# Kernel tuning notes

Hardware: AMD Instinct MI355X
Metric: run time of the kernel (lower is better)

## Reference

```python
import jax, jax.numpy as jnp
import numpy as np

NUM_EMBEDDINGS = 1024
EMBEDDING_DIM = 64
COMMITMENT_COST = 0.25


def setup_inputs() -> dict:
    key = jax.random.key(0)
    k1, k2 = jax.random.split(key)
    z = jax.random.normal(k1, (16, EMBEDDING_DIM, 64, 64), dtype=jnp.float32)
    # nn.Embedding init: uniform(-1/K, 1/K)
    emb = jax.random.uniform(
        k2, (NUM_EMBEDDINGS, EMBEDDING_DIM), dtype=jnp.float32,
        minval=-1.0 / NUM_EMBEDDINGS, maxval=1.0 / NUM_EMBEDDINGS)
    return {"z": z, "emb": emb}


def reference(z, emb):
    # b c h w -> b h w c
    zc = jnp.transpose(z, (0, 2, 3, 1))
    B, H, W, D = zc.shape
    zf = zc.reshape(-1, D)  # [N, D]
    K = emb.shape[0]

    # L2 distances: ||z||^2 + ||e||^2 - 2 z e^T   -> [N, K]
    distances = (jnp.sum(zf * zf, axis=1, keepdims=True)
                 + jnp.sum(emb * emb, axis=1)
                 - 2.0 * jnp.matmul(zf, emb.T))
    encoding_indices = jnp.argmin(distances, axis=1)  # [N]

    # one_hot @ emb  ==  gather
    quantized = emb[encoding_indices].reshape(zc.shape)  # [B,H,W,D]

    reconstruction_errors = jnp.sum((quantized - zc) ** 2, axis=-1).reshape(-1)
    avg_error = jnp.mean(reconstruction_errors)

    e_latent_loss = jnp.mean((jax.lax.stop_gradient(quantized) - zc) ** 2)
    q_latent_loss = jnp.mean((quantized - jax.lax.stop_gradient(zc)) ** 2)
    loss = q_latent_loss + COMMITMENT_COST * e_latent_loss

    # straight-through estimator
    quantized_st = zc + jax.lax.stop_gradient(quantized - zc)
    out = jnp.transpose(quantized_st, (0, 3, 1, 2))  # b h w c -> b c h w

    # perplexity: avg one-hot usage (histogram instead of dense one-hot)
    N = zf.shape[0]
    counts = jnp.zeros((K,), dtype=jnp.float32).at[encoding_indices].add(1.0)
    avg_probs = counts / N
    perplexity = jnp.exp(-jnp.sum(avg_probs * jnp.log(avg_probs + 1e-10)))

    return out, loss, perplexity, avg_error
```

## Files before the change

### kernel.cpp

```cpp
#include <hip/hip_runtime.h>
#include <stdint.h>

#define HW   4096
#define NEMB 1024

typedef float        f32x4  __attribute__((ext_vector_type(4)));
typedef short        h16x8  __attribute__((ext_vector_type(8)));
typedef unsigned int u32x4  __attribute__((ext_vector_type(4)));

#define CVTPKH(D, LO, HI) asm("v_cvt_pkrtz_f16_f32 %0, %1, %2" : "=v"(D) : "v"(LO), "v"(HI))

__device__ __forceinline__ void gload_lds16(const float* g, float* l) {
    __builtin_amdgcn_global_load_lds(
        (const __attribute__((address_space(1))) void*)(uintptr_t)g,
        (__attribute__((address_space(3))) void*)(uintptr_t)l, 16, 0, 0);
}

__global__ __launch_bounds__(128) void vq_init(const float* __restrict__ emb,
                                               unsigned int* __restrict__ counts,
                                               float* __restrict__ errsum,
                                               float* __restrict__ ens,
                                               unsigned int* __restrict__ embw) {
    const int k = blockIdx.x * 128 + threadIdx.x;
    counts[k] = 0u;
    if (k == 0) *errsum = 0.0f;
    const float* e = emb + k * 64;
    float a[8] = {0,0,0,0,0,0,0,0};
    unsigned int* dst = embw + k * 32;
    #pragma unroll
    for (int c = 0; c < 8; ++c) {
        f32x4 v0 = *(const f32x4*)(e + c * 8);
        f32x4 v1 = *(const f32x4*)(e + c * 8 + 4);
        a[0] += v0.x * v0.x; a[1] += v0.y * v0.y;
        a[2] += v0.z * v0.z; a[3] += v0.w * v0.w;
        a[4] += v1.x * v1.x; a[5] += v1.y * v1.y;
        a[6] += v1.z * v1.z; a[7] += v1.w * v1.w;
        u32x4 w;
        CVTPKH(w.x, v0.x, v0.y); CVTPKH(w.y, v0.z, v0.w);
        CVTPKH(w.z, v1.x, v1.y); CVTPKH(w.w, v1.z, v1.w);
        *(u32x4*)&dst[(c ^ (k & 7)) << 2] = w;
    }
    ens[k] = ((a[0]+a[1]) + (a[2]+a[3])) + ((a[4]+a[5]) + (a[6]+a[7]));
}

__global__ __launch_bounds__(512, 4)
void vq_main(const float* __restrict__ z, const float* __restrict__ emb,
             const float* __restrict__ ens, const unsigned int* __restrict__ embw,
             float* __restrict__ out, unsigned int* __restrict__ counts,
             float* __restrict__ errsum)
{
    __shared__ __attribute__((aligned(16))) float z_lds[64 * 128];
    __shared__ __attribute__((aligned(16))) unsigned int et_w[256 * 32];
    __shared__ __attribute__((aligned(16))) float ens_lds[NEMB];
    __shared__ int   idx_sh[128];
    __shared__ float errp[512];

    const int t   = threadIdx.x;
    const int n0  = blockIdx.x * 128;
    const int bb  = n0 >> 12;
    const int hw0 = n0 & 4095;
    const float* zb = z + bb * (64 * HW) + hw0;

    #pragma unroll
    for (int it = 0; it < 4; ++it) {
        const int p = it * 512 + t;
        gload_lds16(zb + (p >> 5) * HW + (p & 31) * 4, z_lds + p * 4);
    }
    if (t < 256) gload_lds16(ens + t * 4, ens_lds + t * 4);
    #pragma unroll
    for (int it = 0; it < 4; ++it) {
        const int p = it * 512 + t;
        gload_lds16((const float*)embw + p * 4, (float*)et_w + p * 4);
    }
    __syncthreads();

    const int l   = t & 63;
    const int wv  = t >> 6;
    const int col = l & 15;
    const int bg  = l >> 4;

    h16x8 a0, a1;
    {
        const int xs = wv * 16 + col;
        u32x4 wa, wb;
        #pragma unroll
        for (int p2 = 0; p2 < 4; ++p2) {
            float lo = z_lds[(bg * 8 + p2 * 2    ) * 128 + xs];
            float hi = z_lds[(bg * 8 + p2 * 2 + 1) * 128 + xs];
            CVTPKH(wa[p2], lo, hi);
            float lo2 = z_lds[(32 + bg * 8 + p2 * 2    ) * 128 + xs];
            float hi2 = z_lds[(32 + bg * 8 + p2 * 2 + 1) * 128 + xs];
            CVTPKH(wb[p2], lo2, hi2);
        }
        a0 = __builtin_bit_cast(h16x8, wa);
        a1 = __builtin_bit_cast(h16x8, wb);
    }

    const int slot0 = bg ^ (col & 7);
    const unsigned int* ep0 = et_w + col * 32 + slot0 * 4;
    const unsigned int* ep1 = et_w + col * 32 + (slot0 ^ 4) * 4;
    const float* ensp = ens_lds + col;

    float mval[4] = {__builtin_inff(), __builtin_inff(), __builtin_inff(), __builtin_inff()};
    int   midx[4] = {0, 0, 0, 0};

    #pragma unroll
    for (int kt = 0; kt < 4; ++kt) {
        #pragma unroll
        for (int i = 0; i < 16; ++i) {
            u32x4 bw0 = *(const u32x4*)(ep0 + i * 512);
            u32x4 bw1 = *(const u32x4*)(ep1 + i * 512);
            float en = ensp[kt * 256 + i * 16];
            f32x4 cc = {0.0f, 0.0f, 0.0f, 0.0f};
            cc = __builtin_amdgcn_mfma_f32_16x16x32_f16(a0, __builtin_bit_cast(h16x8, bw0), cc, 0, 0, 0);
            cc = __builtin_amdgcn_mfma_f32_16x16x32_f16(a1, __builtin_bit_cast(h16x8, bw1), cc, 0, 0, 0);
            const int kg = kt * 256 + i * 16 + col;
            #pragma unroll
            for (int j = 0; j < 4; ++j) {
                const float s = fmaf(-2.0f, cc[j], en);
                if (s < mval[j]) { mval[j] = s; midx[j] = kg; }
            }
        }

        __syncthreads();
        if (kt < 3) {
            const float* src = (const float*)(embw + (kt + 1) * 8192);
            #pragma unroll
            for (int it = 0; it < 4; ++it) {
                const int p = it * 512 + t;
                gload_lds16(src + p * 4, (float*)et_w + p * 4);
            }
            __syncthreads();
        }
    }

    #pragma unroll
    for (int j = 0; j < 4; ++j) {
        float m = mval[j]; int id = midx[j];
        #pragma unroll
        for (int mk = 1; mk <= 8; mk <<= 1) {
            float m2 = __shfl_xor(m, mk, 64);
            int   i2 = __shfl_xor(id, mk, 64);
            if (m2 < m || (m2 == m && i2 < id)) { m = m2; id = i2; }
        }
        if (col == 0) idx_sh[wv * 16 + bg * 4 + j] = id;
    }
    __syncthreads();

    if (t < 128) atomicAdd(&counts[idx_sh[t]], 1u);

    {
        const int x  = t & 127;
        const int cg = t >> 7;
        const int idx = idx_sh[x];
        const float* er = emb + idx * 64;
        float* ob = out + bb * (64 * HW) + hw0 + x;
        float part = 0.0f;
        #pragma unroll
        for (int cq = 0; cq < 4; ++cq) {
            const int c = cg * 16 + cq * 4;
            f32x4 e4 = *(const f32x4*)&er[c];
            float z0 = z_lds[(c+0) * 128 + x];
            float z1 = z_lds[(c+1) * 128 + x];
            float z2 = z_lds[(c+2) * 128 + x];
            float z3 = z_lds[(c+3) * 128 + x];
            ob[(c+0) * HW] = z0 + (e4.x - z0);
            ob[(c+1) * HW] = z1 + (e4.y - z1);
            ob[(c+2) * HW] = z2 + (e4.z - z2);
            ob[(c+3) * HW] = z3 + (e4.w - z3);
            float d0 = z0 - e4.x, d1 = z1 - e4.y, d2 = z2 - e4.z, d3 = z3 - e4.w;
            part = fmaf(d0, d0, part); part = fmaf(d1, d1, part);
            part = fmaf(d2, d2, part); part = fmaf(d3, d3, part);
        }
        errp[t] = part;
    }
    __syncthreads();
    if (t < 128) {
        float s = (errp[t] + errp[t + 128]) + (errp[t + 256] + errp[t + 384]);
        #pragma unroll
        for (int off = 32; off >= 1; off >>= 1) s += __shfl_down(s, off, 64);
        if ((t & 63) == 0) atomicAdd(errsum, s);
    }
}

__global__ __launch_bounds__(256) void vq_fin(const unsigned int* __restrict__ counts,
                                              const float* __restrict__ errsum,
                                              float* __restrict__ scal)
{
    __shared__ float part[4];
    const int t = threadIdx.x;
    float s = 0.0f;
    for (int k = t; k < NEMB; k += 256) {
        float p = (float)counts[k] * (1.0f / 65536.0f);
        s += p * logf(p + 1e-10f);
    }
    #pragma unroll
    for (int off = 32; off >= 1; off >>= 1) s += __shfl_down(s, off, 64);
    if ((t & 63) == 0) part[t >> 6] = s;
    __syncthreads();
    if (t == 0) {
        float tot = (part[0] + part[1]) + (part[2] + part[3]);
        float es  = *errsum;
        scal[0] = 1.25f * (es * (1.0f / 4194304.0f));
        scal[1] = expf(-tot);
        scal[2] = es * (1.0f / 65536.0f);
    }
}

extern "C" void kernel_launch(void* const* d_in, const int* in_sizes, int n_in,
                              void* d_out, int out_size, void* d_ws, size_t ws_size,
                              hipStream_t stream) {
    const float* z   = (const float*)d_in[0];
    const float* emb = (const float*)d_in[1];
    float* out = (float*)d_out;
    unsigned int* counts = (unsigned int*)d_ws;
    float* errsum = (float*)((char*)d_ws + 4096);
    float* ens    = (float*)((char*)d_ws + 8192);
    unsigned int* embw = (unsigned int*)((char*)d_ws + 16384);

    vq_init<<<8, 128, 0, stream>>>(emb, counts, errsum, ens, embw);
    vq_main<<<512, 512, 0, stream>>>(z, emb, ens, embw, out, counts, errsum);
    vq_fin<<<1, 256, 0, stream>>>(counts, errsum, out + 4194304);
}
```

Before: 46.95 us.

## Keep codebook slice in registers per wave and pack argmin into integer keys

Measured after the change: 44.13 us. 1.06x faster.

```diff
diff --git a/kernel.cpp b/kernel.cpp
--- a/kernel.cpp
+++ b/kernel.cpp
@@ -19,14 +19,14 @@
 __global__ __launch_bounds__(128) void vq_init(const float* __restrict__ emb,
                                                unsigned int* __restrict__ counts,
                                                float* __restrict__ errsum,
-                                               float* __restrict__ ens,
-                                               unsigned int* __restrict__ embw) {
+                                               float* __restrict__ ens1,
+                                               unsigned int* __restrict__ embh) {
     const int k = blockIdx.x * 128 + threadIdx.x;
     counts[k] = 0u;
     if (k == 0) *errsum = 0.0f;
     const float* e = emb + k * 64;
+    unsigned int* dst = embh + k * 32;
     float a[8] = {0,0,0,0,0,0,0,0};
-    unsigned int* dst = embw + k * 32;
     #pragma unroll
     for (int c = 0; c < 8; ++c) {
         f32x4 v0 = *(const f32x4*)(e + c * 8);
@@ -38,20 +38,21 @@
         u32x4 w;
         CVTPKH(w.x, v0.x, v0.y); CVTPKH(w.y, v0.z, v0.w);
         CVTPKH(w.z, v1.x, v1.y); CVTPKH(w.w, v1.z, v1.w);
-        *(u32x4*)&dst[(c ^ (k & 7)) << 2] = w;
-    }
-    ens[k] = ((a[0]+a[1]) + (a[2]+a[3])) + ((a[4]+a[5]) + (a[6]+a[7]));
+        *(u32x4*)&dst[c * 4] = w;
+    }
+    ens1[k] = 1.0f + (((a[0]+a[1]) + (a[2]+a[3])) + ((a[4]+a[5]) + (a[6]+a[7])));
 }
 
 __global__ __launch_bounds__(512, 4)
 void vq_main(const float* __restrict__ z, const float* __restrict__ emb,
-             const float* __restrict__ ens, const unsigned int* __restrict__ embw,
+             const float* __restrict__ ens1, const unsigned int* __restrict__ embh,
              float* __restrict__ out, unsigned int* __restrict__ counts,
              float* __restrict__ errsum)
 {
     __shared__ __attribute__((aligned(16))) float z_lds[64 * 128];
-    __shared__ __attribute__((aligned(16))) unsigned int et_w[256 * 32];
+    __shared__ __attribute__((aligned(16))) unsigned int zh[128 * 32];
     __shared__ __attribute__((aligned(16))) float ens_lds[NEMB];
+    __shared__ unsigned int kd[8][128];
     __shared__ int   idx_sh[128];
     __shared__ float errp[512];
 
@@ -66,88 +67,103 @@
         const int p = it * 512 + t;
         gload_lds16(zb + (p >> 5) * HW + (p & 31) * 4, z_lds + p * 4);
     }
-    if (t < 256) gload_lds16(ens + t * 4, ens_lds + t * 4);
-    #pragma unroll
-    for (int it = 0; it < 4; ++it) {
-        const int p = it * 512 + t;
-        gload_lds16((const float*)embw + p * 4, (float*)et_w + p * 4);
-    }
-    __syncthreads();
+    if (t < 256) gload_lds16(ens1 + t * 4, ens_lds + t * 4);
+    __syncthreads();
+
+    {
+        const int x = t & 127;
+        #pragma unroll
+        for (int ss = 0; ss < 2; ++ss) {
+            const int s = (x + (t >> 7) * 2 + ss) & 7;
+            const int c = s ^ (x & 7);
+            u32x4 w;
+            CVTPKH(w.x, z_lds[(8*c + 0) * 128 + x], z_lds[(8*c + 1) * 128 + x]);
+            CVTPKH(w.y, z_lds[(8*c + 2) * 128 + x], z_lds[(8*c + 3) * 128 + x]);
+            CVTPKH(w.z, z_lds[(8*c + 4) * 128 + x], z_lds[(8*c + 5) * 128 + x]);
+            CVTPKH(w.w, z_lds[(8*c + 6) * 128 + x], z_lds[(8*c + 7) * 128 + x]);
+            *(u32x4*)&zh[x * 32 + s * 4] = w;
+        }
+    }
 
     const int l   = t & 63;
     const int wv  = t >> 6;
     const int col = l & 15;
     const int bg  = l >> 4;
 
-    h16x8 a0, a1;
+    u32x4 bw0[8], bw1[8];
     {
-        const int xs = wv * 16 + col;
-        u32x4 wa, wb;
-        #pragma unroll
-        for (int p2 = 0; p2 < 4; ++p2) {
-            float lo = z_lds[(bg * 8 + p2 * 2    ) * 128 + xs];
-            float hi = z_lds[(bg * 8 + p2 * 2 + 1) * 128 + xs];
-            CVTPKH(wa[p2], lo, hi);
-            float lo2 = z_lds[(32 + bg * 8 + p2 * 2    ) * 128 + xs];
-            float hi2 = z_lds[(32 + bg * 8 + p2 * 2 + 1) * 128 + xs];
-            CVTPKH(wb[p2], lo2, hi2);
-        }
-        a0 = __builtin_bit_cast(h16x8, wa);
-        a1 = __builtin_bit_cast(h16x8, wb);
-    }
-
-    const int slot0 = bg ^ (col & 7);
-    const unsigned int* ep0 = et_w + col * 32 + slot0 * 4;
-    const unsigned int* ep1 = et_w + col * 32 + (slot0 ^ 4) * 4;
-    const float* ensp = ens_lds + col;
-
-    float mval[4] = {__builtin_inff(), __builtin_inff(), __builtin_inff(), __builtin_inff()};
-    int   midx[4] = {0, 0, 0, 0};
-
-    #pragma unroll
-    for (int kt = 0; kt < 4; ++kt) {
-        #pragma unroll
-        for (int i = 0; i < 16; ++i) {
-            u32x4 bw0 = *(const u32x4*)(ep0 + i * 512);
-            u32x4 bw1 = *(const u32x4*)(ep1 + i * 512);
-            float en = ensp[kt * 256 + i * 16];
+        const unsigned int* ebase = embh + (wv * 128 + col) * 32 + bg * 4;
+        #pragma unroll
+        for (int g = 0; g < 8; ++g) {
+            bw0[g] = *(const u32x4*)(ebase + g * 16 * 32);
+            bw1[g] = *(const u32x4*)(ebase + g * 16 * 32 + 16);
+        }
+    }
+    float en[8];
+    #pragma unroll
+    for (int g = 0; g < 8; ++g) en[g] = ens_lds[wv * 128 + g * 16 + col];
+
+    __syncthreads();
+
+    const unsigned int lkc = (unsigned int)col;
+    #pragma unroll 1
+    for (int st = 0; st < 8; ++st) {
+        const int xs = st * 16 + col;
+        const int sA = bg ^ (col & 7);
+        u32x4 wa = *(const u32x4*)&zh[xs * 32 + sA * 4];
+        u32x4 wb = *(const u32x4*)&zh[xs * 32 + (sA ^ 4) * 4];
+        h16x8 a0 = __builtin_bit_cast(h16x8, wa);
+        h16x8 a1 = __builtin_bit_cast(h16x8, wb);
+
+        unsigned int k0 = ~0u, k1 = ~0u, k2 = ~0u, k3 = ~0u;
+        #pragma unroll
+        for (int g = 0; g < 8; ++g) {
             f32x4 cc = {0.0f, 0.0f, 0.0f, 0.0f};
-            cc = __builtin_amdgcn_mfma_f32_16x16x32_f16(a0, __builtin_bit_cast(h16x8, bw0), cc, 0, 0, 0);
-            cc = __builtin_amdgcn_mfma_f32_16x16x32_f16(a1, __builtin_bit_cast(h16x8, bw1), cc, 0, 0, 0);
-            const int kg = kt * 256 + i * 16 + col;
-            #pragma unroll
-            for (int j = 0; j < 4; ++j) {
-                const float s = fmaf(-2.0f, cc[j], en);
-                if (s < mval[j]) { mval[j] = s; midx[j] = kg; }
-            }
-        }
-
-        __syncthreads();
-        if (kt < 3) {
-            const float* src = (const float*)(embw + (kt + 1) * 8192);
-            #pragma unroll
-            for (int it = 0; it < 4; ++it) {
-                const int p = it * 512 + t;
-                gload_lds16(src + p * 4, (float*)et_w + p * 4);
-            }
-            __syncthreads();
-        }
-    }
-
-    #pragma unroll
-    for (int j = 0; j < 4; ++j) {
-        float m = mval[j]; int id = midx[j];
+            cc = __builtin_amdgcn_mfma_f32_16x16x32_f16(a0, __builtin_bit_cast(h16x8, bw0[g]), cc, 0, 0, 0);
+            cc = __builtin_amdgcn_mfma_f32_16x16x32_f16(a1, __builtin_bit_cast(h16x8, bw1[g]), cc, 0, 0, 0);
+            const unsigned int lk = (unsigned int)(g << 4) | lkc;
+            float s0 = fmaf(-2.0f, cc[0], en[g]);
+            float s1 = fmaf(-2.0f, cc[1], en[g]);
+            float s2 = fmaf(-2.0f, cc[2], en[g]);
+            float s3 = fmaf(-2.0f, cc[3], en[g]);
+            unsigned int q0 = (__builtin_bit_cast(unsigned int, s0) & ~127u) | lk;
+            unsigned int q1 = (__builtin_bit_cast(unsigned int, s1) & ~127u) | lk;
+            unsigned int q2 = (__builtin_bit_cast(unsigned int, s2) & ~127u) | lk;
+            unsigned int q3 = (__builtin_bit_cast(unsigned int, s3) & ~127u) | lk;
+            k0 = k0 < q0 ? k0 : q0;  k1 = k1 < q1 ? k1 : q1;
+            k2 = k2 < q2 ? k2 : q2;  k3 = k3 < q3 ? k3 : q3;
+        }
         #pragma unroll
         for (int mk = 1; mk <= 8; mk <<= 1) {
-            float m2 = __shfl_xor(m, mk, 64);
-            int   i2 = __shfl_xor(id, mk, 64);
-            if (m2 < m || (m2 == m && i2 < id)) { m = m2; id = i2; }
-        }
-        if (col == 0) idx_sh[wv * 16 + bg * 4 + j] = id;
-    }
-    __syncthreads();
-
-    if (t < 128) atomicAdd(&counts[idx_sh[t]], 1u);
+            unsigned int o0 = (unsigned int)__shfl_xor((int)k0, mk, 64);
+            unsigned int o1 = (unsigned int)__shfl_xor((int)k1, mk, 64);
+            unsigned int o2 = (unsigned int)__shfl_xor((int)k2, mk, 64);
+            unsigned int o3 = (unsigned int)__shfl_xor((int)k3, mk, 64);
+            k0 = k0 < o0 ? k0 : o0;  k1 = k1 < o1 ? k1 : o1;
+            k2 = k2 < o2 ? k2 : o2;  k3 = k3 < o3 ? k3 : o3;
+        }
+        if (col == 0) {
+            u32x4 kv = {k0, k1, k2, k3};
+            *(u32x4*)&kd[wv][st * 16 + bg * 4] = kv;
+        }
+    }
+    __syncthreads();
+
+    if (t < 128) {
+        unsigned int kw = kd[0][t];
+        unsigned int bv = kw & ~127u;
+        int bk = (int)(kw & 127u);
+        #pragma unroll
+        for (int w = 1; w < 8; ++w) {
+            kw = kd[w][t];
+            unsigned int vw = kw & ~127u;
+            int kk = w * 128 + (int)(kw & 127u);
+            if (vw < bv || (vw == bv && kk < bk)) { bv = vw; bk = kk; }
+        }
+        idx_sh[t] = bk;
+        atomicAdd(&counts[bk], 1u);
+    }
+    __syncthreads();
 
     {
         const int x  = t & 127;
@@ -215,10 +231,10 @@
     float* out = (float*)d_out;
     unsigned int* counts = (unsigned int*)d_ws;
     float* errsum = (float*)((char*)d_ws + 4096);
-    float* ens    = (float*)((char*)d_ws + 8192);
-    unsigned int* embw = (unsigned int*)((char*)d_ws + 16384);
-
-    vq_init<<<8, 128, 0, stream>>>(emb, counts, errsum, ens, embw);
-    vq_main<<<512, 512, 0, stream>>>(z, emb, ens, embw, out, counts, errsum);
+    float* ens1   = (float*)((char*)d_ws + 8192);
+    unsigned int* embh = (unsigned int*)((char*)d_ws + 16384);
+
+    vq_init<<<8, 128, 0, stream>>>(emb, counts, errsum, ens1, embh);
+    vq_main<<<512, 512, 0, stream>>>(z, emb, ens1, embh, out, counts, errsum);
     vq_fin<<<1, 256, 0, stream>>>(counts, errsum, out + 4194304);
 }
```
